# Performance work log

Hardware: AMD Instinct MI355X
Metric: run time of the kernel (lower is better)

## Reference

```python
import jax, jax.numpy as jnp
import numpy as np
import math

IN_IMGSIZE = (64, 64)
KERNEL = (3, 3)
STRIDE = (1, 1)


def find_same_padding(in_size, k, s):
    out_size = math.ceil(in_size / s)
    return max((out_size - 1) * s + k - in_size, 0)


def setup_inputs() -> dict:
    key = jax.random.key(0)
    k1, k2 = jax.random.split(key)
    in_ch, out_ch = 128, 256
    B = 32
    X = jax.random.normal(k1, (B, in_ch, IN_IMGSIZE[0], IN_IMGSIZE[1]), dtype=jnp.float32)
    # He-uniform init as in the torch module
    variance = 2.0 / (KERNEL[0] * KERNEL[1] * in_ch)
    bound = math.sqrt(3.0 * variance)
    weights = jax.random.uniform(k2, (out_ch, in_ch, KERNEL[0], KERNEL[1]),
                                 minval=-bound, maxval=bound, dtype=jnp.float32)
    biases = jnp.zeros((out_ch,), dtype=jnp.float32)
    return {"X": X, "weights": weights, "biases": biases}


def reference(X, weights, biases):
    # 'same' padding amounts (height_pad == width_pad here, so torch's
    # F.pad dim-ordering quirk in the original is a no-op)
    hp = find_same_padding(IN_IMGSIZE[0], KERNEL[0], STRIDE[0])
    wp = find_same_padding(IN_IMGSIZE[1], KERNEL[1], STRIDE[1])
    # Replicate torch pad order: first pair of pad_tuple (height halves) pads width,
    # second pair (width halves) pads height. Identical when hp == wp.
    X_pad = jnp.pad(X, ((0, 0), (0, 0),
                        (wp // 2, wp - wp // 2),
                        (hp // 2, hp - hp // 2)))
    # Dense one-hot projector einsum in the original == standard conv2d.
    out = jax.lax.conv_general_dilated(
        X_pad, weights, window_strides=STRIDE, padding='VALID',
        dimension_numbers=('NCHW', 'OIHW', 'NCHW'))
    return out + biases[None, :, None, None]
```

## Files before the change

kernel.cpp:

```cpp
#include <hip/hip_runtime.h>

#define B_N  32
#define CI   128
#define CO   256
#define HH   64
#define WW   64
#define HP   66
#define WP   66
#define KTOT 1152
#define PIX  4096

#define XT_ELEMS ((size_t)B_N * HP * WP * CI)
#define XT_BYTES (XT_ELEMS * 2)
#define WT_ELEMS ((size_t)CO * KTOT)
#define WT_BYTES (WT_ELEMS * 2)
#define WS_NEEDED (XT_BYTES + WT_BYTES)

#define AS1 __attribute__((address_space(1)))
#define AS3 __attribute__((address_space(3)))

typedef unsigned short us;
typedef __attribute__((ext_vector_type(8))) short bf16x8;
typedef __attribute__((ext_vector_type(4))) float f32x4;
typedef __attribute__((ext_vector_type(8))) unsigned short us8;

__device__ __forceinline__ us f2bf(float f) {
    unsigned int u = __builtin_bit_cast(unsigned int, f);
    u += 0x7fffu + ((u >> 16) & 1u);
    return (us)(u >> 16);
}

__device__ __forceinline__ void gload16(const void* g, const void* l) {
    __builtin_amdgcn_global_load_lds((const AS1 unsigned int*)g,
                                     (AS3 unsigned int*)l, 16, 0, 0);
}

__global__ void k_transpose(const float* __restrict__ X, us* __restrict__ Xt) {
    int bh   = blockIdx.x;
    int b    = bh >> 6, h = bh & 63;
    int wv   = threadIdx.x >> 6;
    int lane = threadIdx.x & 63;
    const float* src = X + (((size_t)(b * CI + wv * 32) * HH + h) << 6) + lane;
    us8 v[4];
#pragma unroll
    for (int j = 0; j < 32; ++j)
        v[j >> 3][j & 7] = f2bf(src[(size_t)j << 12]);
    us* dst = Xt + ((size_t)(b * HP + h + 1) * WP + (lane + 1)) * CI + wv * 32;
#pragma unroll
    for (int q = 0; q < 4; ++q)
        *(us8*)(dst + q * 8) = v[q];
    us8 z = (us8)0;
    int t = threadIdx.x;
    if (t < 32) {
        int wcol = (t < 16) ? 0 : 65;
        int i = t & 15;
        *(us8*)(Xt + ((size_t)(b * HP + h + 1) * WP + wcol) * CI + i * 8) = z;
    }
    if (h == 0) {
        for (int i = t; i < WP * CI / 8; i += 256)
            *(us8*)(Xt + (size_t)(b * HP + 0) * WP * CI + (size_t)i * 8) = z;
    }
    if (h == 63) {
        for (int i = t; i < WP * CI / 8; i += 256)
            *(us8*)(Xt + (size_t)(b * HP + 65) * WP * CI + (size_t)i * 8) = z;
    }
}

__global__ void k_prepw(const float* __restrict__ W, us* __restrict__ Wt) {
    int co = blockIdx.x;
    for (int k = threadIdx.x; k < KTOT; k += 256) {
        int tap = k >> 7, ci = k & 127;
        Wt[(size_t)co * KTOT + k] = f2bf(W[((size_t)co * CI + ci) * 9 + tap]);
    }
}

__global__ __launch_bounds__(512, 2) void k_conv_gemm(
    const us* __restrict__ Xt, const us* __restrict__ Wt,
    const float* __restrict__ bias, float* __restrict__ out) {

    __shared__ __attribute__((aligned(16))) us As[2][256 * 64];
    __shared__ __attribute__((aligned(16))) us Bs[2][256 * 64];

    const int bid0 = blockIdx.x;
    const int bid  = (bid0 & 7) * 64 + (bid0 >> 3);
    const int b    = bid >> 4;
    const int nb   = bid & 15;
    const int h0   = nb << 2;

    const int tid  = threadIdx.x;
    const int lane = tid & 63;
    const int wv   = tid >> 6;
    const int lr   = lane & 15, lg = lane >> 4;
    const int wm   = wv >> 2,  wn = wv & 3;

    const int srow = tid >> 3;
    const int sg   = (tid & 7) ^ (srow & 7);

    f32x4 acc[8][4] = {};

    auto stageA = [&](int slot, int t, int qm) {
#pragma unroll
        for (int c = 0; c < 2; ++c) {
            const int r0 = qm * 64 + c * 128;
            const us* src = Wt + (size_t)(r0 + srow) * KTOT + t * 64 + sg * 8;
            const us* d   = &As[slot][(r0 + (wv << 3)) * 64];
            gload16(src, d);
        }
    };
    auto stageB = [&](int slot, int t, int qn) {
        const int tap = t >> 1, ci0 = (t & 1) << 6;
        const int kh = tap / 3, kw = tap - kh * 3;
#pragma unroll
        for (int c = 0; c < 2; ++c) {
            const int r  = qn * 128 + c * 64 + srow;
            const int p  = ((r >> 5) & 3) * 64 + (r >> 7) * 32 + (r & 31);
            const int hh = h0 + (p >> 6) + kh;
            const int wc = (p & 63) + kw;
            const us* src = Xt + ((size_t)(b * HP + hh) * WP + wc) * CI + ci0 + sg * 8;
            const us* d   = &Bs[slot][(qn * 128 + c * 64 + (wv << 3)) * 64];
            gload16(src, d);
        }
    };

    bf16x8 a[4][2], bb[2][2];
    auto ldA = [&](int slot, int qm) {
#pragma unroll
        for (int m = 0; m < 4; ++m)
#pragma unroll
            for (int kk = 0; kk < 2; ++kk) {
                const int row = wm * 128 + qm * 64 + m * 16 + lr;
                const int g   = (kk * 4 + lg) ^ (row & 7);
                a[m][kk] = *(const bf16x8*)&As[slot][row * 64 + g * 8];
            }
    };
    auto ldB = [&](int slot, int qn) {
#pragma unroll
        for (int n = 0; n < 2; ++n)
#pragma unroll
            for (int kk = 0; kk < 2; ++kk) {
                const int r = qn * 128 + wn * 32 + n * 16 + lr;
                const int g = (kk * 4 + lg) ^ (r & 7);
                bb[n][kk] = *(const bf16x8*)&Bs[slot][r * 64 + g * 8];
            }
    };
    auto mma = [&](int qm, int qn) {
        __builtin_amdgcn_s_setprio(1);
#pragma unroll
        for (int kk = 0; kk < 2; ++kk)
#pragma unroll
            for (int m = 0; m < 4; ++m)
#pragma unroll
                for (int n = 0; n < 2; ++n)
                    acc[qm * 4 + m][qn * 2 + n] = __builtin_amdgcn_mfma_f32_16x16x32_bf16(
                        a[m][kk], bb[n][kk], acc[qm * 4 + m][qn * 2 + n], 0, 0, 0);
        __builtin_amdgcn_s_setprio(0);
    };

    stageA(0, 0, 0);
    stageB(0, 0, 0);
    stageA(0, 0, 1);
    stageB(0, 0, 1);

    for (int t = 0; t < 18; ++t) {
        const int s = t & 1, ns = s ^ 1;
        const int tn = (t < 17) ? t + 1 : 17;
        asm volatile("s_waitcnt vmcnt(4)" ::: "memory");
        __builtin_amdgcn_s_barrier();
        stageA(ns, tn, 0);
        ldA(s, 0); ldB(s, 0);
        mma(0, 0);
        asm volatile("s_waitcnt vmcnt(4)" ::: "memory");
        __builtin_amdgcn_s_barrier();
        stageB(ns, tn, 0);
        ldA(s, 1);
        mma(1, 0);
        asm volatile("s_waitcnt vmcnt(4)" ::: "memory");
        __builtin_amdgcn_s_barrier();
        stageA(ns, tn, 1);
        ldB(s, 1);
        mma(1, 1);
        stageB(ns, tn, 1);
        ldA(s, 0);
        mma(0, 1);
    }

    const int p0base = nb * 256 + wn * 64;
#pragma unroll
    for (int mf = 0; mf < 8; ++mf) {
        const int qm = mf >> 2, m = mf & 3;
#pragma unroll
        for (int j = 0; j < 4; ++j) {
            const int co = wm * 128 + qm * 64 + m * 16 + lg * 4 + j;
            const float bv = bias[co];
            float* op = out + ((size_t)(b * CO + co) << 12) + p0base + lr;
#pragma unroll
            for (int nf = 0; nf < 4; ++nf) {
                const int qn = nf >> 1, n = nf & 1;
                op[qn * 32 + n * 16] = acc[mf][nf][j] + bv;
            }
        }
    }
}

__global__ void k_naive(const float* __restrict__ X, const float* __restrict__ W,
                        const float* __restrict__ bias, float* __restrict__ out) {
    long idx = (long)blockIdx.x * blockDim.x + threadIdx.x;
    if (idx >= (long)B_N * CO * PIX) return;
    int p = idx & 4095, co = (int)((idx >> 12) & 255), b = (int)(idx >> 20);
    int h = p >> 6, w = p & 63;
    float s = bias[co];
    for (int ci = 0; ci < CI; ++ci) {
        const float* xp = X + ((size_t)(b * CI + ci) << 12);
        const float* wp = W + ((size_t)(co * CI + ci)) * 9;
        for (int kh = 0; kh < 3; ++kh) {
            int hh2 = h + kh - 1; if ((unsigned)hh2 >= 64u) continue;
            for (int kw = 0; kw < 3; ++kw) {
                int ww2 = w + kw - 1; if ((unsigned)ww2 >= 64u) continue;
                s += xp[(hh2 << 6) + ww2] * wp[kh * 3 + kw];
            }
        }
    }
    out[idx] = s;
}

extern "C" void kernel_launch(void* const* d_in, const int* in_sizes, int n_in,
                              void* d_out, int out_size, void* d_ws, size_t ws_size,
                              hipStream_t stream) {
    const float* X    = (const float*)d_in[0];
    const float* W    = (const float*)d_in[1];
    const float* bias = (const float*)d_in[2];
    float* out = (float*)d_out;

    if (ws_size < WS_NEEDED) {
        long total = (long)B_N * CO * PIX;
        k_naive<<<(int)((total + 255) / 256), 256, 0, stream>>>(X, W, bias, out);
        return;
    }

    us* Xt = (us*)d_ws;
    us* Wt = (us*)((char*)d_ws + XT_BYTES);

    k_transpose<<<B_N * HH, 256, 0, stream>>>(X, Xt);
    k_prepw<<<CO, 256, 0, stream>>>(W, Wt);
    k_conv_gemm<<<512, 512, 0, stream>>>(Xt, Wt, bias, out);
}
```

Before: 119.0 us.

## Restructure conv GEMM pipeline with split-K LDS halves and merge prep kernels

Merges the input transpose and weight conversion into a single launch, removing one kernel launch. Reorganizes the implicit-GEMM main loop so the B tile is stored as two 32-channel halves with a new swizzle. Loads are issued two K-steps ahead, and the loop runs finer-grained ldA/ldB/mma phases with more barriers and sched_barrier fences. The deeper prefetch is meant to hide global-load latency, at the cost of more barrier synchronization and a more fragile buffer reuse schedule.

Measured after the change: 139.4 us. 1.17x slower.

```diff
diff --git a/kernel.cpp b/kernel.cpp
--- a/kernel.cpp
+++ b/kernel.cpp
@@ -3,8 +3,6 @@
 #define B_N  32
 #define CI   128
 #define CO   256
-#define HH   64
-#define WW   64
 #define HP   66
 #define WP   66
 #define KTOT 1152
@@ -12,8 +10,7 @@
 
 #define XT_ELEMS ((size_t)B_N * HP * WP * CI)
 #define XT_BYTES (XT_ELEMS * 2)
-#define WT_ELEMS ((size_t)CO * KTOT)
-#define WT_BYTES (WT_ELEMS * 2)
+#define WT_BYTES ((size_t)CO * KTOT * 2)
 #define WS_NEEDED (XT_BYTES + WT_BYTES)
 
 #define AS1 __attribute__((address_space(1)))
@@ -35,12 +32,23 @@
                                      (AS3 unsigned int*)l, 16, 0, 0);
 }
 
-__global__ void k_transpose(const float* __restrict__ X, us* __restrict__ Xt) {
+__global__ void k_prep(const float* __restrict__ X, const float* __restrict__ W,
+                       us* __restrict__ Xt, us* __restrict__ Wt) {
+    if (blockIdx.x >= 2048) {
+        int base = (blockIdx.x - 2048) * (64 * KTOT);
+        for (int idx = threadIdx.x; idx < 64 * KTOT; idx += 256) {
+            int g = base + idx;
+            int co = g / KTOT, k = g - co * KTOT;
+            int tap = k >> 7, ci = k & 127;
+            Wt[g] = f2bf(W[((size_t)co * CI + ci) * 9 + tap]);
+        }
+        return;
+    }
     int bh   = blockIdx.x;
     int b    = bh >> 6, h = bh & 63;
     int wv   = threadIdx.x >> 6;
     int lane = threadIdx.x & 63;
-    const float* src = X + (((size_t)(b * CI + wv * 32) * HH + h) << 6) + lane;
+    const float* src = X + (((size_t)(b * CI + wv * 32) * 64 + h) << 6) + lane;
     us8 v[4];
 #pragma unroll
     for (int j = 0; j < 32; ++j)
@@ -56,22 +64,12 @@
         int i = t & 15;
         *(us8*)(Xt + ((size_t)(b * HP + h + 1) * WP + wcol) * CI + i * 8) = z;
     }
-    if (h == 0) {
+    if (h == 0)
         for (int i = t; i < WP * CI / 8; i += 256)
             *(us8*)(Xt + (size_t)(b * HP + 0) * WP * CI + (size_t)i * 8) = z;
-    }
-    if (h == 63) {
+    if (h == 63)
         for (int i = t; i < WP * CI / 8; i += 256)
             *(us8*)(Xt + (size_t)(b * HP + 65) * WP * CI + (size_t)i * 8) = z;
-    }
-}
-
-__global__ void k_prepw(const float* __restrict__ W, us* __restrict__ Wt) {
-    int co = blockIdx.x;
-    for (int k = threadIdx.x; k < KTOT; k += 256) {
-        int tap = k >> 7, ci = k & 127;
-        Wt[(size_t)co * KTOT + k] = f2bf(W[((size_t)co * CI + ci) * 9 + tap]);
-    }
 }
 
 __global__ __launch_bounds__(512, 2) void k_conv_gemm(
@@ -79,7 +77,7 @@
     const float* __restrict__ bias, float* __restrict__ out) {
 
     __shared__ __attribute__((aligned(16))) us As[2][256 * 64];
-    __shared__ __attribute__((aligned(16))) us Bs[2][256 * 64];
+    __shared__ __attribute__((aligned(16))) us Bs[2][2][256 * 32];
 
     const int bid0 = blockIdx.x;
     const int bid  = (bid0 & 7) * 64 + (bid0 >> 3);
@@ -93,111 +91,108 @@
     const int lr   = lane & 15, lg = lane >> 4;
     const int wm   = wv >> 2,  wn = wv & 3;
 
-    const int srow = tid >> 3;
-    const int sg   = (tid & 7) ^ (srow & 7);
-
     f32x4 acc[8][4] = {};
-
-    auto stageA = [&](int slot, int t, int qm) {
+    bf16x8 a[8], bb[2];
+
+    auto stageA = [&](int slot, int t) {
+        const int srow = tid >> 3;
+        const int sg   = (tid & 7) ^ (srow & 7);
+#pragma unroll
+        for (int c = 0; c < 4; ++c) {
+            const int r = c * 64 + srow;
+            gload16(Wt + (size_t)r * KTOT + t * 64 + sg * 8,
+                    &As[slot][(c * 64 + (wv << 3)) * 64]);
+        }
+    };
+    auto stageB = [&](int slot, int t, int u) {
+        const int srow = tid >> 2;
+        const int sg   = (tid & 3) ^ ((srow >> 1) & 3);
+        const int tap  = t >> 1;
+        const int tkh  = tap / 3, tkw = tap - tkh * 3;
+        const int ci   = ((t & 1) << 6) + (u << 5) + (sg << 3);
 #pragma unroll
         for (int c = 0; c < 2; ++c) {
-            const int r0 = qm * 64 + c * 128;
-            const us* src = Wt + (size_t)(r0 + srow) * KTOT + t * 64 + sg * 8;
-            const us* d   = &As[slot][(r0 + (wv << 3)) * 64];
-            gload16(src, d);
-        }
-    };
-    auto stageB = [&](int slot, int t, int qn) {
-        const int tap = t >> 1, ci0 = (t & 1) << 6;
-        const int kh = tap / 3, kw = tap - kh * 3;
-#pragma unroll
-        for (int c = 0; c < 2; ++c) {
-            const int r  = qn * 128 + c * 64 + srow;
-            const int p  = ((r >> 5) & 3) * 64 + (r >> 7) * 32 + (r & 31);
-            const int hh = h0 + (p >> 6) + kh;
-            const int wc = (p & 63) + kw;
-            const us* src = Xt + ((size_t)(b * HP + hh) * WP + wc) * CI + ci0 + sg * 8;
-            const us* d   = &Bs[slot][(qn * 128 + c * 64 + (wv << 3)) * 64];
-            gload16(src, d);
-        }
-    };
-
-    bf16x8 a[4][2], bb[2][2];
-    auto ldA = [&](int slot, int qm) {
-#pragma unroll
-        for (int m = 0; m < 4; ++m)
-#pragma unroll
-            for (int kk = 0; kk < 2; ++kk) {
-                const int row = wm * 128 + qm * 64 + m * 16 + lr;
-                const int g   = (kk * 4 + lg) ^ (row & 7);
-                a[m][kk] = *(const bf16x8*)&As[slot][row * 64 + g * 8];
-            }
-    };
-    auto ldB = [&](int slot, int qn) {
-#pragma unroll
-        for (int n = 0; n < 2; ++n)
-#pragma unroll
-            for (int kk = 0; kk < 2; ++kk) {
-                const int r = qn * 128 + wn * 32 + n * 16 + lr;
-                const int g = (kk * 4 + lg) ^ (r & 7);
-                bb[n][kk] = *(const bf16x8*)&Bs[slot][r * 64 + g * 8];
-            }
-    };
-    auto mma = [&](int qm, int qn) {
+            const int p  = c * 128 + srow;
+            const int hh = h0 + (p >> 6) + tkh;
+            const int wc = (p & 63) + tkw;
+            gload16(Xt + ((size_t)(b * HP + hh) * WP + wc) * CI + ci,
+                    &Bs[slot][u][(c * 128 + (wv << 4)) * 32]);
+        }
+    };
+    auto ldA = [&](int slot, int kk) {
+#pragma unroll
+        for (int m = 0; m < 8; ++m) {
+            const int row = wm * 128 + m * 16 + lr;
+            const int g   = ((kk << 2) + lg) ^ (row & 7);
+            a[m] = *(const bf16x8*)&As[slot][row * 64 + g * 8];
+        }
+    };
+    auto ldB = [&](int slot, int u, int nh) {
+#pragma unroll
+        for (int n = 0; n < 2; ++n) {
+            const int p = wn * 64 + (nh * 2 + n) * 16 + lr;
+            const int g = lg ^ ((p >> 1) & 3);
+            bb[n] = *(const bf16x8*)&Bs[slot][u][p * 32 + g * 8];
+        }
+    };
+    auto mma = [&](int nh) {
         __builtin_amdgcn_s_setprio(1);
 #pragma unroll
-        for (int kk = 0; kk < 2; ++kk)
-#pragma unroll
-            for (int m = 0; m < 4; ++m)
-#pragma unroll
-                for (int n = 0; n < 2; ++n)
-                    acc[qm * 4 + m][qn * 2 + n] = __builtin_amdgcn_mfma_f32_16x16x32_bf16(
-                        a[m][kk], bb[n][kk], acc[qm * 4 + m][qn * 2 + n], 0, 0, 0);
+        for (int m = 0; m < 8; ++m)
+#pragma unroll
+            for (int n = 0; n < 2; ++n)
+                acc[m][nh * 2 + n] = __builtin_amdgcn_mfma_f32_16x16x32_bf16(
+                    a[m], bb[n], acc[m][nh * 2 + n], 0, 0, 0);
         __builtin_amdgcn_s_setprio(0);
-    };
-
-    stageA(0, 0, 0);
+        __builtin_amdgcn_sched_barrier(0);
+    };
+
     stageB(0, 0, 0);
-    stageA(0, 0, 1);
     stageB(0, 0, 1);
+    stageA(0, 0);
+    stageB(1, 1, 0);
+    stageA(1, 1);
+    asm volatile("s_waitcnt vmcnt(6)" ::: "memory");
+    __builtin_amdgcn_s_barrier();
 
     for (int t = 0; t < 18; ++t) {
-        const int s = t & 1, ns = s ^ 1;
-        const int tn = (t < 17) ? t + 1 : 17;
-        asm volatile("s_waitcnt vmcnt(4)" ::: "memory");
-        __builtin_amdgcn_s_barrier();
-        stageA(ns, tn, 0);
-        ldA(s, 0); ldB(s, 0);
-        mma(0, 0);
-        asm volatile("s_waitcnt vmcnt(4)" ::: "memory");
-        __builtin_amdgcn_s_barrier();
-        stageB(ns, tn, 0);
-        ldA(s, 1);
-        mma(1, 0);
-        asm volatile("s_waitcnt vmcnt(4)" ::: "memory");
-        __builtin_amdgcn_s_barrier();
-        stageA(ns, tn, 1);
-        ldB(s, 1);
-        mma(1, 1);
-        stageB(ns, tn, 1);
-        ldA(s, 0);
-        mma(0, 1);
-    }
-
-    const int p0base = nb * 256 + wn * 64;
-#pragma unroll
-    for (int mf = 0; mf < 8; ++mf) {
-        const int qm = mf >> 2, m = mf & 3;
+        const int s  = t & 1, ns = s ^ 1;
+        const int t1 = (t + 1 < 18) ? t + 1 : 17;
+        const int t2 = (t + 2 < 18) ? t + 2 : 17;
+        ldA(s, 0); ldB(s, 0, 0);
+        stageB(ns, t1, 1);
+        __builtin_amdgcn_s_barrier();
+        mma(0);
+        __builtin_amdgcn_s_barrier();
+        ldB(s, 0, 1);
+        __builtin_amdgcn_s_barrier();
+        mma(1);
+        asm volatile("s_waitcnt vmcnt(8)" ::: "memory");
+        __builtin_amdgcn_s_barrier();
+        ldA(s, 1); ldB(s, 1, 0);
+        stageB(s, t2, 0);
+        __builtin_amdgcn_s_barrier();
+        mma(0);
+        __builtin_amdgcn_s_barrier();
+        ldB(s, 1, 1);
+        stageA(s, t2);
+        __builtin_amdgcn_s_barrier();
+        mma(1);
+        asm volatile("s_waitcnt vmcnt(8)" ::: "memory");
+        __builtin_amdgcn_s_barrier();
+    }
+
+    const int p0 = nb * 256 + wn * 64;
+#pragma unroll
+    for (int mi = 0; mi < 8; ++mi) {
 #pragma unroll
         for (int j = 0; j < 4; ++j) {
-            const int co = wm * 128 + qm * 64 + m * 16 + lg * 4 + j;
+            const int co = wm * 128 + mi * 16 + lg * 4 + j;
             const float bv = bias[co];
-            float* op = out + ((size_t)(b * CO + co) << 12) + p0base + lr;
-#pragma unroll
-            for (int nf = 0; nf < 4; ++nf) {
-                const int qn = nf >> 1, n = nf & 1;
-                op[qn * 32 + n * 16] = acc[mf][nf][j] + bv;
-            }
+            float* op = out + ((size_t)(b * CO + co) << 12) + p0 + lr;
+#pragma unroll
+            for (int ni = 0; ni < 4; ++ni)
+                op[ni * 16] = acc[mi][ni][j] + bv;
         }
     }
 }
@@ -240,7 +235,6 @@
     us* Xt = (us*)d_ws;
     us* Wt = (us*)((char*)d_ws + XT_BYTES);
 
-    k_transpose<<<B_N * HH, 256, 0, stream>>>(X, Xt);
-    k_prepw<<<CO, 256, 0, stream>>>(W, Wt);
+    k_prep<<<2052, 256, 0, stream>>>(X, W, Xt, Wt);
     k_conv_gemm<<<512, 512, 0, stream>>>(Xt, Wt, bias, out);
 }
```

## Fuse weight prep into transpose and restructure GEMM pipeline with deeper prefetch

Applied to the files above, without the earlier changes.

Folds the weight-conversion kernel into the input transpose kernel, removing one launch. Reworks the conv GEMM main loop into a 256-row-split, ping-pong schedule: each iteration interleaves LDS fragment loads, prefetches of half-tiles two steps ahead and MFMA blocks, with explicit lgkmcnt waits and barriers around each quarter. Also changes the output pixel mapping and lowers launch_bounds occupancy to 1 block per CU. The extra barriers and the lower occupancy hint could offset the deeper prefetch.

Result: faster. 107.0 us (-10.1%).

```diff
diff --git a/kernel.cpp b/kernel.cpp
--- a/kernel.cpp
+++ b/kernel.cpp
@@ -3,8 +3,6 @@
 #define B_N  32
 #define CI   128
 #define CO   256
-#define HH   64
-#define WW   64
 #define HP   66
 #define WP   66
 #define KTOT 1152
@@ -12,8 +10,7 @@
 
 #define XT_ELEMS ((size_t)B_N * HP * WP * CI)
 #define XT_BYTES (XT_ELEMS * 2)
-#define WT_ELEMS ((size_t)CO * KTOT)
-#define WT_BYTES (WT_ELEMS * 2)
+#define WT_BYTES ((size_t)CO * KTOT * 2)
 #define WS_NEEDED (XT_BYTES + WT_BYTES)
 
 #define AS1 __attribute__((address_space(1)))
@@ -35,12 +32,13 @@
                                      (AS3 unsigned int*)l, 16, 0, 0);
 }
 
-__global__ void k_transpose(const float* __restrict__ X, us* __restrict__ Xt) {
+__global__ void k_transpose(const float* __restrict__ X, const float* __restrict__ W,
+                            us* __restrict__ Xt, us* __restrict__ Wt) {
     int bh   = blockIdx.x;
     int b    = bh >> 6, h = bh & 63;
     int wv   = threadIdx.x >> 6;
     int lane = threadIdx.x & 63;
-    const float* src = X + (((size_t)(b * CI + wv * 32) * HH + h) << 6) + lane;
+    const float* src = X + (((size_t)(b * CI + wv * 32) * 64 + h) << 6) + lane;
     us8 v[4];
 #pragma unroll
     for (int j = 0; j < 32; ++j)
@@ -49,32 +47,30 @@
 #pragma unroll
     for (int q = 0; q < 4; ++q)
         *(us8*)(dst + q * 8) = v[q];
+
+    int t = threadIdx.x;
+    if (t < 144) {
+        int g   = bh * 144 + t;
+        int co  = g / KTOT, k = g - co * KTOT;
+        int tap = k >> 7, ci = k & 127;
+        Wt[g] = f2bf(W[((size_t)co * CI + ci) * 9 + tap]);
+    }
+
     us8 z = (us8)0;
-    int t = threadIdx.x;
     if (t < 32) {
         int wcol = (t < 16) ? 0 : 65;
         int i = t & 15;
         *(us8*)(Xt + ((size_t)(b * HP + h + 1) * WP + wcol) * CI + i * 8) = z;
     }
-    if (h == 0) {
+    if (h == 0)
         for (int i = t; i < WP * CI / 8; i += 256)
             *(us8*)(Xt + (size_t)(b * HP + 0) * WP * CI + (size_t)i * 8) = z;
-    }
-    if (h == 63) {
+    if (h == 63)
         for (int i = t; i < WP * CI / 8; i += 256)
             *(us8*)(Xt + (size_t)(b * HP + 65) * WP * CI + (size_t)i * 8) = z;
-    }
-}
-
-__global__ void k_prepw(const float* __restrict__ W, us* __restrict__ Wt) {
-    int co = blockIdx.x;
-    for (int k = threadIdx.x; k < KTOT; k += 256) {
-        int tap = k >> 7, ci = k & 127;
-        Wt[(size_t)co * KTOT + k] = f2bf(W[((size_t)co * CI + ci) * 9 + tap]);
-    }
-}
-
-__global__ __launch_bounds__(512, 2) void k_conv_gemm(
+}
+
+__global__ __launch_bounds__(512, 1) void k_conv_gemm(
     const us* __restrict__ Xt, const us* __restrict__ Wt,
     const float* __restrict__ bias, float* __restrict__ out) {
 
@@ -82,9 +78,9 @@
     __shared__ __attribute__((aligned(16))) us Bs[2][256 * 64];
 
     const int bid0 = blockIdx.x;
-    const int bid  = (bid0 & 7) * 64 + (bid0 >> 3);
-    const int b    = bid >> 4;
-    const int nb   = bid & 15;
+    const int wg   = (bid0 & 7) * 64 + (bid0 >> 3);
+    const int b    = wg >> 4;
+    const int nb   = wg & 15;
     const int h0   = nb << 2;
 
     const int tid  = threadIdx.x;
@@ -97,53 +93,53 @@
     const int sg   = (tid & 7) ^ (srow & 7);
 
     f32x4 acc[8][4] = {};
-
-    auto stageA = [&](int slot, int t, int qm) {
+    bf16x8 a[4][2];
+    bf16x8 bb[2][2][2];
+
+    auto stageA = [&](int slot, int t, int h) {
 #pragma unroll
         for (int c = 0; c < 2; ++c) {
-            const int r0 = qm * 64 + c * 128;
-            const us* src = Wt + (size_t)(r0 + srow) * KTOT + t * 64 + sg * 8;
-            const us* d   = &As[slot][(r0 + (wv << 3)) * 64];
-            gload16(src, d);
-        }
-    };
-    auto stageB = [&](int slot, int t, int qn) {
-        const int tap = t >> 1, ci0 = (t & 1) << 6;
-        const int kh = tap / 3, kw = tap - kh * 3;
+            const int row = h * 128 + c * 64 + srow;
+            gload16(Wt + (size_t)row * KTOT + t * 64 + sg * 8,
+                    &As[slot][(h * 128 + c * 64 + (wv << 3)) * 64]);
+        }
+    };
+    auto stageB = [&](int slot, int t, int h) {
+        const int tap = t >> 1;
+        const int kh  = tap / 3, kw = tap - kh * 3;
+        const int ci0 = (t & 1) << 6;
 #pragma unroll
         for (int c = 0; c < 2; ++c) {
-            const int r  = qn * 128 + c * 64 + srow;
-            const int p  = ((r >> 5) & 3) * 64 + (r >> 7) * 32 + (r & 31);
+            const int p  = h * 128 + c * 64 + srow;
             const int hh = h0 + (p >> 6) + kh;
             const int wc = (p & 63) + kw;
-            const us* src = Xt + ((size_t)(b * HP + hh) * WP + wc) * CI + ci0 + sg * 8;
-            const us* d   = &Bs[slot][(qn * 128 + c * 64 + (wv << 3)) * 64];
-            gload16(src, d);
-        }
-    };
-
-    bf16x8 a[4][2], bb[2][2];
-    auto ldA = [&](int slot, int qm) {
+            gload16(Xt + ((size_t)(b * HP + hh) * WP + wc) * CI + ci0 + sg * 8,
+                    &Bs[slot][(h * 128 + c * 64 + (wv << 3)) * 64]);
+        }
+    };
+    auto ldA = [&](int slot, int mh) {
 #pragma unroll
         for (int m = 0; m < 4; ++m)
 #pragma unroll
             for (int kk = 0; kk < 2; ++kk) {
-                const int row = wm * 128 + qm * 64 + m * 16 + lr;
-                const int g   = (kk * 4 + lg) ^ (row & 7);
+                const int row = mh * 128 + wm * 64 + m * 16 + lr;
+                const int g   = ((kk << 2) + lg) ^ (row & 7);
                 a[m][kk] = *(const bf16x8*)&As[slot][row * 64 + g * 8];
             }
     };
-    auto ldB = [&](int slot, int qn) {
+    auto ldB = [&](int slot, int nh) {
 #pragma unroll
         for (int n = 0; n < 2; ++n)
 #pragma unroll
             for (int kk = 0; kk < 2; ++kk) {
-                const int r = qn * 128 + wn * 32 + n * 16 + lr;
-                const int g = (kk * 4 + lg) ^ (r & 7);
-                bb[n][kk] = *(const bf16x8*)&Bs[slot][r * 64 + g * 8];
-            }
-    };
-    auto mma = [&](int qm, int qn) {
+                const int row = nh * 128 + wn * 32 + n * 16 + lr;
+                const int g   = ((kk << 2) + lg) ^ (row & 7);
+                bb[nh][n][kk] = *(const bf16x8*)&Bs[slot][row * 64 + g * 8];
+            }
+    };
+    auto mma = [&](int mh, int nh) {
+        asm volatile("s_waitcnt lgkmcnt(0)" ::: "memory");
+        __builtin_amdgcn_sched_barrier(0);
         __builtin_amdgcn_s_setprio(1);
 #pragma unroll
         for (int kk = 0; kk < 2; ++kk)
@@ -151,52 +147,55 @@
             for (int m = 0; m < 4; ++m)
 #pragma unroll
                 for (int n = 0; n < 2; ++n)
-                    acc[qm * 4 + m][qn * 2 + n] = __builtin_amdgcn_mfma_f32_16x16x32_bf16(
-                        a[m][kk], bb[n][kk], acc[qm * 4 + m][qn * 2 + n], 0, 0, 0);
+                    acc[mh * 4 + m][nh * 2 + n] = __builtin_amdgcn_mfma_f32_16x16x32_bf16(
+                        a[m][kk], bb[nh][n][kk], acc[mh * 4 + m][nh * 2 + n], 0, 0, 0);
         __builtin_amdgcn_s_setprio(0);
     };
 
-    stageA(0, 0, 0);
-    stageB(0, 0, 0);
-    stageA(0, 0, 1);
-    stageB(0, 0, 1);
-
+    stageA(0, 0, 0); stageB(0, 0, 0); stageB(0, 0, 1); stageA(0, 0, 1);
+    stageA(1, 1, 0); stageB(1, 1, 0); stageB(1, 1, 1);
+    asm volatile("s_waitcnt vmcnt(6)" ::: "memory");
+    __builtin_amdgcn_s_barrier();
+
+#pragma unroll
     for (int t = 0; t < 18; ++t) {
         const int s = t & 1, ns = s ^ 1;
-        const int tn = (t < 17) ? t + 1 : 17;
-        asm volatile("s_waitcnt vmcnt(4)" ::: "memory");
-        __builtin_amdgcn_s_barrier();
-        stageA(ns, tn, 0);
         ldA(s, 0); ldB(s, 0);
+        if (t + 1 < 18) stageA(ns, t + 1, 1);
+        __builtin_amdgcn_s_barrier();
         mma(0, 0);
-        asm volatile("s_waitcnt vmcnt(4)" ::: "memory");
-        __builtin_amdgcn_s_barrier();
-        stageB(ns, tn, 0);
+        __builtin_amdgcn_s_barrier();
+        ldB(s, 1);
+        if (t + 2 < 18) stageA(s, t + 2, 0);
+        __builtin_amdgcn_s_barrier();
+        mma(0, 1);
+        __builtin_amdgcn_s_barrier();
         ldA(s, 1);
+        if (t + 2 < 18) stageB(s, t + 2, 0);
+        __builtin_amdgcn_s_barrier();
+        mma(1, 1);
+        __builtin_amdgcn_s_barrier();
+        if (t + 2 < 18) stageB(s, t + 2, 1);
+        __builtin_amdgcn_s_barrier();
         mma(1, 0);
-        asm volatile("s_waitcnt vmcnt(4)" ::: "memory");
-        __builtin_amdgcn_s_barrier();
-        stageA(ns, tn, 1);
-        ldB(s, 1);
-        mma(1, 1);
-        stageB(ns, tn, 1);
-        ldA(s, 0);
-        mma(0, 1);
-    }
-
-    const int p0base = nb * 256 + wn * 64;
+        if (t < 16)       asm volatile("s_waitcnt vmcnt(6)" ::: "memory");
+        else if (t == 16) asm volatile("s_waitcnt vmcnt(0)" ::: "memory");
+        __builtin_amdgcn_s_barrier();
+    }
+
+    const int p0 = nb * 256;
 #pragma unroll
     for (int mf = 0; mf < 8; ++mf) {
-        const int qm = mf >> 2, m = mf & 3;
+        const int mh = mf >> 2, m = mf & 3;
 #pragma unroll
         for (int j = 0; j < 4; ++j) {
-            const int co = wm * 128 + qm * 64 + m * 16 + lg * 4 + j;
+            const int co = mh * 128 + wm * 64 + m * 16 + lg * 4 + j;
             const float bv = bias[co];
-            float* op = out + ((size_t)(b * CO + co) << 12) + p0base + lr;
+            float* op = out + ((size_t)(b * CO + co) << 12) + p0 + wn * 32 + lr;
 #pragma unroll
             for (int nf = 0; nf < 4; ++nf) {
-                const int qn = nf >> 1, n = nf & 1;
-                op[qn * 32 + n * 16] = acc[mf][nf][j] + bv;
+                const int nh = nf >> 1, n = nf & 1;
+                op[nh * 128 + n * 16] = acc[mf][nf][j] + bv;
             }
         }
     }
@@ -240,7 +239,6 @@
     us* Xt = (us*)d_ws;
     us* Wt = (us*)((char*)d_ws + XT_BYTES);
 
-    k_transpose<<<B_N * HH, 256, 0, stream>>>(X, Xt);
-    k_prepw<<<CO, 256, 0, stream>>>(W, Wt);
+    k_transpose<<<B_N * 64, 256, 0, stream>>>(X, W, Xt, Wt);
     k_conv_gemm<<<512, 512, 0, stream>>>(Xt, Wt, bias, out);
 }
```
